# Optimization experiments

Hardware: AMD Instinct MI355X
Metric: run time of the kernel (lower is better)

The kernel has to match this reference:

```python
import jax, jax.numpy as jnp
import numpy as np

N_NODES = 50000
N_EDGES = 600000
D = 128
APPNP_K = 5
APPNP_ALPHA = 0.2


def _mish(x):
    return x * jnp.tanh(jax.nn.softplus(x))


def setup_inputs() -> dict:
    key = jax.random.key(0)
    ks = jax.random.split(key, 6)
    x = jax.random.normal(ks[0], (N_NODES, D), dtype=jnp.float32)
    src = jax.random.randint(ks[1], (N_EDGES,), 0, N_NODES, dtype=jnp.int32)
    dst = jax.random.randint(ks[2], (N_EDGES,), 0, N_NODES, dtype=jnp.int32)
    W1 = jax.random.normal(ks[3], (D, D), dtype=jnp.float32) * (1.0 / np.sqrt(D))
    b1 = jnp.zeros((D,), dtype=jnp.float32)
    W2 = jax.random.normal(ks[4], (2 * D, D), dtype=jnp.float32) * (1.0 / np.sqrt(2 * D))
    b2 = jnp.zeros((D,), dtype=jnp.float32)
    eps1 = jnp.zeros((1,), dtype=jnp.float32)
    eps2 = jnp.zeros((1,), dtype=jnp.float32)
    return {"x": x, "src": src, "dst": dst, "W1": W1, "b1": b1,
            "W2": W2, "b2": b2, "eps1": eps1, "eps2": eps2}


def _appnp(x0, src, dst):
    # DGL APPNPConv: symmetric degree normalization, k power-iteration steps.
    ones = jnp.ones((src.shape[0],), dtype=x0.dtype)
    deg_out = jnp.clip(jax.ops.segment_sum(ones, src, num_segments=N_NODES), 1.0)
    deg_in = jnp.clip(jax.ops.segment_sum(ones, dst, num_segments=N_NODES), 1.0)
    norm_o = deg_out[:, None] ** -0.5  # [N,1]
    norm_i = deg_in[:, None] ** -0.5
    h = x0
    for _ in range(APPNP_K):
        h = h * norm_o
        h = jax.ops.segment_sum(h[src], dst, num_segments=N_NODES)  # gather-scatter
        h = h * norm_i
        h = (1.0 - APPNP_ALPHA) * h + APPNP_ALPHA * x0
    return h


def _gin(h, src, dst, eps, W, b):
    # GINConv(sum, learn_eps): (1+eps)*h + sum_{j in N(i)} h_j, then Linear.
    agg = jax.ops.segment_sum(h[src], dst, num_segments=N_NODES)
    return ((1.0 + eps) * h + agg) @ W + b


def reference(x, src, dst, W1, b1, W2, b2, eps1, eps2):
    out = jnp.tanh(x)           # GCNNorm affects edge weights only; node feats then tanh
    x0 = out                    # res_out[0]
    out = _appnp(out, src, dst)
    out = _gin(out, src, dst, eps1[0], W1, b1)          # layer 0
    out = jnp.concatenate([out, x0], axis=1)            # residual concat
    out = _gin(out, src, dst, eps2[0], W2, b2)          # layer 1
    return _mish(out)
```

## Files before the change

### kernel.cpp

```cpp
#include <hip/hip_runtime.h>
#include <hip/hip_fp16.h>
#include <math.h>

#define NN 50000
#define NE 600000
#define NT ((NN + 31) / 32)

#define HB 64
#define HBINS 12500

typedef _Float16 half8_t __attribute__((ext_vector_type(8)));
typedef float f32x16 __attribute__((ext_vector_type(16)));
typedef float f32x2 __attribute__((ext_vector_type(2)));

union F2H { float2 f; __half2 h[2]; };

__device__ __forceinline__ float2 fp8_dec(unsigned short u) {
  f32x2 v = __builtin_amdgcn_cvt_pk_f32_fp8((unsigned int)u, false);
  float2 r; r.x = v.x; r.y = v.y; return r;
}
__device__ __forceinline__ unsigned short fp8_enc(float a, float b) {
  return (unsigned short)__builtin_amdgcn_cvt_pk_fp8_f32(a, b, 0u, false);
}


__global__ __launch_bounds__(256) void k_tanh(const float* __restrict__ x,
                                              const float* __restrict__ no,
                                              __half2* __restrict__ x0h,
                                              unsigned int* __restrict__ x0n8,
                                              unsigned int* __restrict__ x0p8) {
  int i = blockIdx.x * 256 + threadIdx.x;
  if (i >= NN * 32) return;
  float4 v = reinterpret_cast<const float4*>(x)[i];
  float t[4];
  float vv[4] = {v.x, v.y, v.z, v.w};
  #pragma unroll
  for (int j = 0; j < 4; ++j) {
    float xc = fminf(fmaxf(vv[j], -9.f), 9.f);
    float E = __expf(2.f * xc);
    t[j] = (E - 1.f) / (E + 1.f);
  }
  float s = no[i >> 5];
  F2H a;
  a.h[0] = __floats2half2_rn(t[0], t[1]);
  a.h[1] = __floats2half2_rn(t[2], t[3]);
  reinterpret_cast<float2*>(x0h)[i] = a.f;
  unsigned int p = __builtin_amdgcn_cvt_pk_fp8_f32(t[0] * s, t[1] * s, 0u, false);
  p = __builtin_amdgcn_cvt_pk_fp8_f32(t[2] * s, t[3] * s, p, true);
  x0n8[i] = p;
  unsigned int q = __builtin_amdgcn_cvt_pk_fp8_f32(t[0], t[1], 0u, false);
  q = __builtin_amdgcn_cvt_pk_fp8_f32(t[2], t[3], q, true);
  x0p8[i] = q;
}

__global__ __launch_bounds__(256) void k_wt(const float* __restrict__ W1,
                                            const float* __restrict__ W2,
                                            _Float16* __restrict__ w1p,
                                            _Float16* __restrict__ w2p) {
  int i = blockIdx.x * 256 + threadIdx.x;
  if (i < 128 * 128) {
    int k = i >> 7, n = i & 127;
    int nb = n >> 5, r = n & 31, ks = k >> 4, g = (k & 15) >> 3, j = k & 7;
    w1p[(((ks << 2) + nb) * 64 + (g << 5) + r) * 8 + j] = (_Float16)W1[i];
  } else {
    int q = i - 128 * 128;
    if (q < 256 * 128) {
      int k = q >> 7, n = q & 127;
      int nb = n >> 5, r = n & 31, ks = k >> 4, g = (k & 15) >> 3, j = k & 7;
      w2p[(((ks << 2) + nb) * 64 + (g << 5) + r) * 8 + j] = (_Float16)W2[q];
    }
  }
}

__global__ __launch_bounds__(1024) void k_hist(const int* __restrict__ src,
                                               const int* __restrict__ dst,
                                               int* __restrict__ hpart,
                                               int* __restrict__ lseq) {
  __shared__ int lh[HBINS];
  #pragma unroll 1
  for (int ph = 0; ph < 8; ++ph) {
    const int* idx = (ph & 4) ? dst : src;
    int base = (ph & 3) * HBINS;
    for (int i = threadIdx.x; i < HBINS; i += 1024) lh[i] = 0;
    __syncthreads();
    if (ph & 4) {
      for (int e = blockIdx.x * 1024 + threadIdx.x; e < NE; e += HB * 1024) {
        int v = idx[e] - base;
        if ((unsigned)v < (unsigned)HBINS) lseq[e] = atomicAdd(&lh[v], 1);
      }
    } else {
      for (int e = blockIdx.x * 1024 + threadIdx.x; e < NE; e += HB * 1024) {
        int v = idx[e] - base;
        if ((unsigned)v < (unsigned)HBINS) atomicAdd(&lh[v], 1);
      }
    }
    __syncthreads();
    int* outp = hpart + ((size_t)ph * HB + blockIdx.x) * HBINS;
    for (int i = threadIdx.x; i < HBINS; i += 1024) outp[i] = lh[i];
    __syncthreads();
  }
}

__global__ __launch_bounds__(256) void k_merge(int* __restrict__ hpart,
                                               int* __restrict__ ci,
                                               float* __restrict__ no,
                                               float* __restrict__ ni) {
  int i = blockIdx.x * 256 + threadIdx.x;
  if (i >= NN) return;
  int r = i / HBINS, bin = i - r * HBINS;
  const int* ps = hpart + ((size_t)(0 + r) * HB) * HBINS + bin;
  int* pd = hpart + ((size_t)(4 + r) * HB) * HBINS + bin;
  int so = 0, si = 0;
  #pragma unroll 8
  for (int b = 0; b < HB; ++b) so += ps[(size_t)b * HBINS];
  #pragma unroll 8
  for (int b = 0; b < HB; ++b) {
    int* p = pd + (size_t)b * HBINS;
    int t = *p;
    *p = si;
    si += t;
  }
  ci[i] = si;
  no[i] = rsqrtf((float)max(so, 1));
  ni[i] = rsqrtf((float)max(si, 1));
}

__global__ __launch_bounds__(1024) void k_scanA(const int* __restrict__ deg,
                                                int* __restrict__ incl,
                                                int* __restrict__ bsum) {
  int tid = threadIdx.x;
  int gid = blockIdx.x * 1024 + tid;
  int v = (gid < NN) ? deg[gid] : 0;
  int lane = tid & 63;
  #pragma unroll
  for (int o = 1; o < 64; o <<= 1) {
    int n = __shfl_up(v, o);
    if (lane >= o) v += n;
  }
  __shared__ int ws[16];
  int wid = tid >> 6;
  if (lane == 63) ws[wid] = v;
  __syncthreads();
  if (tid < 16) {
    int s = ws[tid];
    #pragma unroll
    for (int o = 1; o < 16; o <<= 1) {
      int n = __shfl_up(s, o);
      if (tid >= o) s += n;
    }
    ws[tid] = s;
  }
  __syncthreads();
  if (wid > 0) v += ws[wid - 1];
  if (gid < NN) incl[gid] = v;
  if (tid == 1023) bsum[blockIdx.x] = v;
}

__global__ __launch_bounds__(64) void k_scanB(const int* __restrict__ bsum,
                                              int* __restrict__ boff, int nb) {
  int t = threadIdx.x;
  int v = (t < nb) ? bsum[t] : 0;
  int orig = v;
  #pragma unroll
  for (int o = 1; o < 64; o <<= 1) {
    int n = __shfl_up(v, o);
    if (t >= o) v += n;
  }
  if (t < nb) boff[t] = v - orig;
}

__global__ __launch_bounds__(256) void k_scanC(const int* __restrict__ incl,
                                               const int* __restrict__ deg,
                                               const int* __restrict__ boff,
                                               int* __restrict__ rp) {
  int i = blockIdx.x * 256 + threadIdx.x;
  if (i < NN) rp[i] = incl[i] - deg[i] + boff[i >> 10];
  if (i == 0) rp[NN] = NE;
}

__global__ __launch_bounds__(256) void k_scatter(const int* __restrict__ src,
                                                 const int* __restrict__ dst,
                                                 const int* __restrict__ lseq,
                                                 const int* __restrict__ hpart,
                                                 const int* __restrict__ rp,
                                                 int* __restrict__ colsrc) {
  int e = blockIdx.x * 256 + threadIdx.x;
  if (e >= NE) return;
  int d = dst[e];
  int r = d / HBINS, bin = d - r * HBINS;
  int b = (e >> 10) & (HB - 1);
  int ofs = hpart[((size_t)(4 + r) * HB + b) * HBINS + bin];
  colsrc[rp[d] + ofs + lseq[e]] = src[e];
}

#define GATHER_LOOP(LOADEXPR)                                        \
  for (int base = 0; base < cnt; base += 64) {                      \
    int e = beg + base + lane;                                      \
    int cv = (e < end) ? cs[e] : 0;                                 \
    int m = cnt - base; if (m > 64) m = 64;                         \
    int j = 0;                                                      \
    for (; j + 8 <= m; j += 8) {                                    \
      _Pragma("unroll")                                             \
      for (int u = 0; u < 8; ++u) {                                 \
        int s = __builtin_amdgcn_readlane(cv, j + u);               \
        LOADEXPR;                                                   \
      }                                                             \
    }                                                               \
    if (j + 4 <= m) {                                               \
      _Pragma("unroll")                                             \
      for (int u = 0; u < 4; ++u) {                                 \
        int s = __builtin_amdgcn_readlane(cv, j + u);               \
        LOADEXPR;                                                   \
      }                                                             \
      j += 4;                                                       \
    }                                                               \
    if (j + 2 <= m) {                                               \
      _Pragma("unroll")                                             \
      for (int u = 0; u < 2; ++u) {                                 \
        int s = __builtin_amdgcn_readlane(cv, j + u);               \
        LOADEXPR;                                                   \
      }                                                             \
      j += 2;                                                       \
    }                                                               \
    if (j < m) {                                                    \
      int s = __builtin_amdgcn_readlane(cv, j);                     \
      LOADEXPR;                                                     \
    }                                                               \
  }

template <bool LAST>
__global__ __launch_bounds__(256) void k_appnp8(const unsigned short* __restrict__ h8,
                                                const __half2* __restrict__ x0,
                                                const float* __restrict__ no,
                                                const float* __restrict__ ni,
                                                const int* __restrict__ rp,
                                                const int* __restrict__ cs,
                                                unsigned short* __restrict__ out8,
                                                __half2* __restrict__ out16) {
  int w = (blockIdx.x * 256 + threadIdx.x) >> 6;
  int lane = threadIdx.x & 63;
  if (w >= NN) return;
  const unsigned short* hl = h8 + lane;
  int beg = rp[w], end = rp[w + 1], cnt = end - beg;
  float ax = 0.f, ay = 0.f;
  GATHER_LOOP({
    float2 f = fp8_dec(hl[s * 64]);
    ax += f.x; ay += f.y;
  })
  float wi = 0.8f * ni[w];
  float2 xv = __half22float2(x0[w * 64 + lane]);
  float rx = wi * ax + 0.2f * xv.x;
  float ry = wi * ay + 0.2f * xv.y;
  if (LAST) {
    out16[w * 64 + lane] = __floats2half2_rn(rx, ry);
  } else {
    float sc = no[w];
    out8[w * 64 + lane] = fp8_enc(rx * sc, ry * sc);
  }
}

__device__ inline void store_packed(_Float16* __restrict__ zp, int w, int lane,
                                    float v0, float v1) {
  int t = w >> 5, r = w & 31;
  int ks = lane >> 3, g = (lane >> 2) & 1, j = (lane & 3) * 2;
  size_t addr = (((size_t)t * 8 + ks) * 64 + g * 32 + r) * 8 + j;
  *reinterpret_cast<__half2*>(zp + addr) = __floats2half2_rn(v0, v1);
}

__global__ __launch_bounds__(256) void k_appnp_first8(const unsigned short* __restrict__ xn8,
                                                      const unsigned short* __restrict__ xp8,
                                                      const __half2* __restrict__ xp,
                                                      const float* __restrict__ epsp,
                                                      const float* __restrict__ no,
                                                      const float* __restrict__ ni,
                                                      const int* __restrict__ rp,
                                                      const int* __restrict__ cs,
                                                      unsigned short* __restrict__ hout8,
                                                      _Float16* __restrict__ zxout) {
  int w = (blockIdx.x * 256 + threadIdx.x) >> 6;
  int lane = threadIdx.x & 63;
  if (w >= NN) return;
  const unsigned short* xnl = xn8 + lane;
  const unsigned short* xpl = xp8 + lane;
  int beg = rp[w], end = rp[w + 1], cnt = end - beg;
  float ax = 0.f, ay = 0.f, bx = 0.f, by = 0.f;
  GATHER_LOOP({
    float2 f = fp8_dec(xnl[s * 64]);
    float2 g2 = fp8_dec(xpl[s * 64]);
    ax += f.x; ay += f.y; bx += g2.x; by += g2.y;
  })
  float2 xv = __half22float2(xp[w * 64 + lane]);
  float wi = 0.8f * ni[w];
  float sc = no[w];
  hout8[w * 64 + lane] = fp8_enc(sc * (wi * ax + 0.2f * xv.x),
                                 sc * (wi * ay + 0.2f * xv.y));
  float e2 = 1.0f + epsp[0];
  store_packed(zxout, w, lane, e2 * xv.x + bx, e2 * xv.y + by);
}

__global__ __launch_bounds__(256) void k_gather_z(const __half2* __restrict__ h,
                                                  const float* __restrict__ epsp,
                                                  const int* __restrict__ rp,
                                                  const int* __restrict__ cs,
                                                  _Float16* __restrict__ zout) {
  int w = (blockIdx.x * 256 + threadIdx.x) >> 6;
  int lane = threadIdx.x & 63;
  if (w >= NN) return;
  const __half2* hl = h + lane;
  int beg = rp[w], end = rp[w + 1], cnt = end - beg;
  float ax = 0.f, ay = 0.f;
  GATHER_LOOP({
    float2 f = __half22float2(hl[s * 64]);
    ax += f.x; ay += f.y;
  })
  float e1 = 1.0f + epsp[0];
  float2 hv = __half22float2(h[w * 64 + lane]);
  store_packed(zout, w, lane, e1 * hv.x + ax, e1 * hv.y + ay);
}

template <int KTOT, bool MISH>
__global__ __launch_bounds__(64) void k_mgemm(const _Float16* __restrict__ z0,
                                              const _Float16* __restrict__ z1,
                                              const _Float16* __restrict__ wp,
                                              const float* __restrict__ bias,
                                              float* __restrict__ outf,
                                              __half2* __restrict__ outh) {
  int lane = threadIdx.x;
  int t = blockIdx.x;
  int row0 = t * 32;
  if (row0 >= NN) return;
  int r31 = lane & 31, g = lane >> 5;
  f32x16 acc[4];
  #pragma unroll
  for (int i = 0; i < 4; ++i) acc[i] = (f32x16)(0.0f);
  #pragma unroll 4
  for (int ks = 0; ks < KTOT / 16; ++ks) {
    const _Float16* zp = (KTOT == 256 && ks >= 8) ? z1 : z0;
    int kls = (KTOT == 256) ? (ks & 7) : ks;
    half8_t a = *reinterpret_cast<const half8_t*>(
        zp + (((size_t)t * 8 + kls) * 64 + lane) * 8);
    #pragma unroll
    for (int nb = 0; nb < 4; ++nb) {
      half8_t b = *reinterpret_cast<const half8_t*>(
          wp + (((size_t)ks * 4 + nb) * 64 + lane) * 8);
      acc[nb] = __builtin_amdgcn_mfma_f32_32x32x16_f16(a, b, acc[nb], 0, 0, 0);
    }
  }
  #pragma unroll
  for (int nb = 0; nb < 4; ++nb) {
    float bv = bias[nb * 32 + r31];
    #pragma unroll
    for (int r = 0; r < 16; ++r) {
      int rl = (r & 3) + 8 * (r >> 2) + 4 * g;
      int grow = row0 + rl;
      if (grow < NN) {
        float v = acc[nb][r] + bv;
        if (MISH) {
          float E = __expf(v);
          float q = E * (E + 2.f);
          float mv = v * q / (q + 2.f);
          v = (v > 15.f) ? v : mv;
          outf[(size_t)grow * 128 + nb * 32 + r31] = v;
        } else {
          float u = __shfl_xor(v, 1);
          if (!(lane & 1)) {
            outh[((size_t)grow * 128 + nb * 32 + r31) >> 1] = __floats2half2_rn(v, u);
          }
        }
      }
    }
  }
}

extern "C" void kernel_launch(void* const* d_in, const int* in_sizes, int n_in,
                              void* d_out, int out_size, void* d_ws, size_t ws_size,
                              hipStream_t stream) {
  const float* x = (const float*)d_in[0];
  const int* src = (const int*)d_in[1];
  const int* dst = (const int*)d_in[2];
  const float* W1 = (const float*)d_in[3];
  const float* b1 = (const float*)d_in[4];
  const float* W2 = (const float*)d_in[5];
  const float* b2 = (const float*)d_in[6];
  const float* eps1 = (const float*)d_in[7];
  const float* eps2 = (const float*)d_in[8];
  float* out = (float*)d_out;

  char* ws = (char*)d_ws;
  size_t off = 0;
  auto alloc = [&](size_t bytes) -> void* {
    void* p = ws + off;
    off += (bytes + 255) & ~(size_t)255;
    return p;
  };
  const size_t NDP = (size_t)NT * 4096;
  __half2* x0h = (__half2*)alloc(NDP * 2);
  unsigned short* x0n8 = (unsigned short*)alloc(NDP);
  unsigned short* x0p8 = (unsigned short*)alloc(NDP);
  unsigned short* hA8 = (unsigned short*)alloc(NDP);
  unsigned short* hB8 = (unsigned short*)alloc(NDP);
  __half2* h5 = (__half2*)alloc(NDP * 2);
  __half2* zx = (__half2*)alloc(NDP * 2);
  __half2* z1p = (__half2*)alloc(NDP * 2);
  __half2* g1h = (__half2*)alloc(NDP * 2);
  __half2* zg = (__half2*)alloc(NDP * 2);
  _Float16* w1p = (_Float16*)alloc(128 * 128 * 2);
  _Float16* w2p = (_Float16*)alloc(256 * 128 * 2);
  int* ci = (int*)alloc(NN * 4);
  float* nrm_o = (float*)alloc(NN * 4);
  float* nrm_i = (float*)alloc(NN * 4);
  int* incl = (int*)alloc(NN * 4);
  int* bsum = (int*)alloc(64 * 4);
  int* boff = (int*)alloc(64 * 4);
  int* rp = (int*)alloc((NN + 1) * 4);
  int* lseq = (int*)alloc(NE * 4);
  int* colsrc = (int*)alloc(NE * 4);

  int* hpart = (int*)zx;

  k_hist<<<HB, 1024, 0, stream>>>(src, dst, hpart, lseq);
  k_merge<<<(NN + 255) / 256, 256, 0, stream>>>(hpart, ci, nrm_o, nrm_i);

  const int SB = (NN + 1023) / 1024;
  k_scanA<<<SB, 1024, 0, stream>>>(ci, incl, bsum);
  k_scanB<<<1, 64, 0, stream>>>(bsum, boff, SB);
  k_scanC<<<(NN + 255) / 256, 256, 0, stream>>>(incl, ci, boff, rp);
  const int EB = (NE + 255) / 256;
  k_scatter<<<EB, 256, 0, stream>>>(src, dst, lseq, hpart, rp, colsrc);

  k_tanh<<<(NN * 32 + 255) / 256, 256, 0, stream>>>(x, nrm_o, x0h,
                                                    (unsigned int*)x0n8,
                                                    (unsigned int*)x0p8);
  k_wt<<<192, 256, 0, stream>>>(W1, W2, w1p, w2p);

  const int GB = (NN * 64 + 255) / 256;
  k_appnp_first8<<<GB, 256, 0, stream>>>(x0n8, x0p8, x0h, eps2, nrm_o, nrm_i,
                                         rp, colsrc, hA8, (_Float16*)zx);
  k_appnp8<false><<<GB, 256, 0, stream>>>(hA8, x0h, nrm_o, nrm_i, rp, colsrc,
                                          hB8, nullptr);
  k_appnp8<false><<<GB, 256, 0, stream>>>(hB8, x0h, nrm_o, nrm_i, rp, colsrc,
                                          hA8, nullptr);
  k_appnp8<false><<<GB, 256, 0, stream>>>(hA8, x0h, nrm_o, nrm_i, rp, colsrc,
                                          hB8, nullptr);
  k_appnp8<true><<<GB, 256, 0, stream>>>(hB8, x0h, nrm_o, nrm_i, rp, colsrc,
                                         nullptr, h5);

  k_gather_z<<<GB, 256, 0, stream>>>(h5, eps1, rp, colsrc, (_Float16*)z1p);

  k_mgemm<128, false><<<NT, 64, 0, stream>>>((const _Float16*)z1p, nullptr, w1p, b1,
                                             nullptr, g1h);
  k_gather_z<<<GB, 256, 0, stream>>>(g1h, eps2, rp, colsrc, (_Float16*)zg);
  k_mgemm<256, true><<<NT, 64, 0, stream>>>((const _Float16*)zg, (const _Float16*)zx,
                                            w2p, b2, out, nullptr);
}
```

Measured before the change: 288.2 us.

## Pack two 16-bit degree counters per LDS word; split GIN gathers into feature halves

The histogram now packs counts for two node ranges into the high and low 16-bit halves of each shared-memory word. This covers all nodes in 2 passes instead of 8, reducing repeated edge-array reads and LDS zeroing, and the merge and scatter kernels are updated to unpack the halves. The GIN neighbour gather is split into two launches over feature halves, each wave handling two nodes with 32 lanes apiece, so each gathered row is 128 bytes and the per-launch working set is smaller. The risk is 16-bit counter overflow if any per-block count reaches 65536, plus divergence and wasted lanes when the two paired nodes have very different degrees.

```diff
diff --git a/kernel.cpp b/kernel.cpp
--- a/kernel.cpp
+++ b/kernel.cpp
@@ -7,7 +7,7 @@
 #define NT ((NN + 31) / 32)
 
 #define HB 64
-#define HBINS 12500
+#define NBIN2 25000
 
 typedef _Float16 half8_t __attribute__((ext_vector_type(8)));
 typedef float f32x16 __attribute__((ext_vector_type(16)));
@@ -72,57 +72,65 @@
   }
 }
 
-__global__ __launch_bounds__(1024) void k_hist(const int* __restrict__ src,
-                                               const int* __restrict__ dst,
-                                               int* __restrict__ hpart,
-                                               int* __restrict__ lseq) {
-  __shared__ int lh[HBINS];
+__global__ __launch_bounds__(1024) void k_hist2(const int* __restrict__ src,
+                                                const int* __restrict__ dst,
+                                                unsigned int* __restrict__ hpart,
+                                                int* __restrict__ lseq) {
+  __shared__ unsigned int lh[NBIN2];
   #pragma unroll 1
-  for (int ph = 0; ph < 8; ++ph) {
-    const int* idx = (ph & 4) ? dst : src;
-    int base = (ph & 3) * HBINS;
-    for (int i = threadIdx.x; i < HBINS; i += 1024) lh[i] = 0;
+  for (int ph = 0; ph < 2; ++ph) {
+    const int* idx = ph ? dst : src;
+    for (int i = threadIdx.x; i < NBIN2; i += 1024) lh[i] = 0;
     __syncthreads();
-    if (ph & 4) {
+    if (ph) {
       for (int e = blockIdx.x * 1024 + threadIdx.x; e < NE; e += HB * 1024) {
-        int v = idx[e] - base;
-        if ((unsigned)v < (unsigned)HBINS) lseq[e] = atomicAdd(&lh[v], 1);
+        int v = idx[e];
+        int hi = (v >= NBIN2) ? 1 : 0;
+        int bin = v - hi * NBIN2;
+        unsigned int old = atomicAdd(&lh[bin], hi ? 65536u : 1u);
+        lseq[e] = (int)((old >> (hi * 16)) & 0xffffu);
       }
     } else {
       for (int e = blockIdx.x * 1024 + threadIdx.x; e < NE; e += HB * 1024) {
-        int v = idx[e] - base;
-        if ((unsigned)v < (unsigned)HBINS) atomicAdd(&lh[v], 1);
+        int v = idx[e];
+        int hi = (v >= NBIN2) ? 1 : 0;
+        atomicAdd(&lh[v - hi * NBIN2], hi ? 65536u : 1u);
       }
     }
     __syncthreads();
-    int* outp = hpart + ((size_t)ph * HB + blockIdx.x) * HBINS;
-    for (int i = threadIdx.x; i < HBINS; i += 1024) outp[i] = lh[i];
+    unsigned int* outp = hpart + ((size_t)ph * HB + blockIdx.x) * NBIN2;
+    for (int i = threadIdx.x; i < NBIN2; i += 1024) outp[i] = lh[i];
     __syncthreads();
   }
 }
 
-__global__ __launch_bounds__(256) void k_merge(int* __restrict__ hpart,
-                                               int* __restrict__ ci,
-                                               float* __restrict__ no,
-                                               float* __restrict__ ni) {
-  int i = blockIdx.x * 256 + threadIdx.x;
-  if (i >= NN) return;
-  int r = i / HBINS, bin = i - r * HBINS;
-  const int* ps = hpart + ((size_t)(0 + r) * HB) * HBINS + bin;
-  int* pd = hpart + ((size_t)(4 + r) * HB) * HBINS + bin;
-  int so = 0, si = 0;
-  #pragma unroll 8
-  for (int b = 0; b < HB; ++b) so += ps[(size_t)b * HBINS];
+__global__ __launch_bounds__(256) void k_merge2(unsigned int* __restrict__ hpart,
+                                                int* __restrict__ ci,
+                                                float* __restrict__ no,
+                                                float* __restrict__ ni) {
+  int bin = blockIdx.x * 256 + threadIdx.x;
+  if (bin >= NBIN2) return;
+  const unsigned int* ps = hpart + bin;
+  unsigned int* pd = hpart + (size_t)HB * NBIN2 + bin;
+  unsigned int so0 = 0, so1 = 0, si0 = 0, si1 = 0;
   #pragma unroll 8
   for (int b = 0; b < HB; ++b) {
-    int* p = pd + (size_t)b * HBINS;
-    int t = *p;
-    *p = si;
-    si += t;
-  }
-  ci[i] = si;
-  no[i] = rsqrtf((float)max(so, 1));
-  ni[i] = rsqrtf((float)max(si, 1));
+    unsigned int v = ps[(size_t)b * NBIN2];
+    so0 += v & 0xffffu; so1 += v >> 16;
+  }
+  #pragma unroll 8
+  for (int b = 0; b < HB; ++b) {
+    unsigned int* p = pd + (size_t)b * NBIN2;
+    unsigned int v = *p;
+    *p = si0 | (si1 << 16);
+    si0 += v & 0xffffu; si1 += v >> 16;
+  }
+  ci[bin] = (int)si0;
+  ci[bin + NBIN2] = (int)si1;
+  no[bin] = rsqrtf((float)max((int)so0, 1));
+  no[bin + NBIN2] = rsqrtf((float)max((int)so1, 1));
+  ni[bin] = rsqrtf((float)max((int)si0, 1));
+  ni[bin + NBIN2] = rsqrtf((float)max((int)si1, 1));
 }
 
 __global__ __launch_bounds__(1024) void k_scanA(const int* __restrict__ deg,
@@ -181,15 +189,17 @@
 __global__ __launch_bounds__(256) void k_scatter(const int* __restrict__ src,
                                                  const int* __restrict__ dst,
                                                  const int* __restrict__ lseq,
-                                                 const int* __restrict__ hpart,
+                                                 const unsigned int* __restrict__ hpart,
                                                  const int* __restrict__ rp,
                                                  int* __restrict__ colsrc) {
   int e = blockIdx.x * 256 + threadIdx.x;
   if (e >= NE) return;
   int d = dst[e];
-  int r = d / HBINS, bin = d - r * HBINS;
+  int hi = (d >= NBIN2) ? 1 : 0;
+  int bin = d - hi * NBIN2;
   int b = (e >> 10) & (HB - 1);
-  int ofs = hpart[((size_t)(4 + r) * HB + b) * HBINS + bin];
+  unsigned int w = hpart[((size_t)HB + b) * NBIN2 + bin];
+  int ofs = (int)((w >> (hi * 16)) & 0xffffu);
   colsrc[rp[d] + ofs + lseq[e]] = src[e];
 }
 
@@ -298,24 +308,47 @@
   store_packed(zxout, w, lane, e2 * xv.x + bx, e2 * xv.y + by);
 }
 
-__global__ __launch_bounds__(256) void k_gather_z(const __half2* __restrict__ h,
-                                                  const float* __restrict__ epsp,
-                                                  const int* __restrict__ rp,
-                                                  const int* __restrict__ cs,
-                                                  _Float16* __restrict__ zout) {
-  int w = (blockIdx.x * 256 + threadIdx.x) >> 6;
+__global__ __launch_bounds__(256) void k_gz_pair(const __half2* __restrict__ h,
+                                                 const float* __restrict__ epsp,
+                                                 const int* __restrict__ rp,
+                                                 const int* __restrict__ cs,
+                                                 _Float16* __restrict__ zout,
+                                                 int hf) {
+  int wp = (blockIdx.x * 256 + threadIdx.x) >> 6;
+  if (wp >= NN / 2) return;
   int lane = threadIdx.x & 63;
-  if (w >= NN) return;
-  const __half2* hl = h + lane;
+  int l31 = lane & 31;
+  int w = wp * 2 + (lane >> 5);
+  const __half2* hl = h + hf * 32 + l31;
   int beg = rp[w], end = rp[w + 1], cnt = end - beg;
   float ax = 0.f, ay = 0.f;
-  GATHER_LOOP({
-    float2 f = __half22float2(hl[s * 64]);
-    ax += f.x; ay += f.y;
-  })
+  for (int base = 0;; base += 32) {
+    int m = cnt - base;
+    if (m > 32) m = 32;
+    int mA = __shfl(m, 0), mB = __shfl(m, 32);
+    int mmax = mA > mB ? mA : mB;
+    if (mmax <= 0) break;
+    int cv = (base + l31 < cnt) ? cs[beg + base + l31] : 0;
+    int j = 0;
+#define PSTEP(U) { int s = __shfl(cv, j + (U), 32);                    \
+                   float2 f = __half22float2(hl[(size_t)s * 64]);      \
+                   if (j + (U) < m) { ax += f.x; ay += f.y; } }
+    for (; j + 8 <= mmax; j += 8) {
+      PSTEP(0) PSTEP(1) PSTEP(2) PSTEP(3) PSTEP(4) PSTEP(5) PSTEP(6) PSTEP(7)
+    }
+    if (j + 4 <= mmax) { PSTEP(0) PSTEP(1) PSTEP(2) PSTEP(3) j += 4; }
+    if (j + 2 <= mmax) { PSTEP(0) PSTEP(1) j += 2; }
+    if (j < mmax) { PSTEP(0) }
+#undef PSTEP
+  }
   float e1 = 1.0f + epsp[0];
-  float2 hv = __half22float2(h[w * 64 + lane]);
-  store_packed(zout, w, lane, e1 * hv.x + ax, e1 * hv.y + ay);
+  float2 hv = __half22float2(h[(size_t)w * 64 + hf * 32 + l31]);
+  int k0 = hf * 64 + l31 * 2;
+  int t = w >> 5, r = w & 31;
+  int ks = k0 >> 4, g = (k0 >> 3) & 1, jj = k0 & 7;
+  size_t addr = (((size_t)t * 8 + ks) * 64 + g * 32 + r) * 8 + jj;
+  *reinterpret_cast<__half2*>(zout + addr) =
+      __floats2half2_rn(e1 * hv.x + ax, e1 * hv.y + ay);
 }
 
 template <int KTOT, bool MISH>
@@ -416,10 +449,10 @@
   int* lseq = (int*)alloc(NE * 4);
   int* colsrc = (int*)alloc(NE * 4);
 
-  int* hpart = (int*)zx;
-
-  k_hist<<<HB, 1024, 0, stream>>>(src, dst, hpart, lseq);
-  k_merge<<<(NN + 255) / 256, 256, 0, stream>>>(hpart, ci, nrm_o, nrm_i);
+  unsigned int* hpart = (unsigned int*)zx;
+
+  k_hist2<<<HB, 1024, 0, stream>>>(src, dst, hpart, lseq);
+  k_merge2<<<(NBIN2 + 255) / 256, 256, 0, stream>>>(hpart, ci, nrm_o, nrm_i);
 
   const int SB = (NN + 1023) / 1024;
   k_scanA<<<SB, 1024, 0, stream>>>(ci, incl, bsum);
@@ -434,6 +467,7 @@
   k_wt<<<192, 256, 0, stream>>>(W1, W2, w1p, w2p);
 
   const int GB = (NN * 64 + 255) / 256;
+  const int GP = (NN / 2 * 64 + 255) / 256;
   k_appnp_first8<<<GB, 256, 0, stream>>>(x0n8, x0p8, x0h, eps2, nrm_o, nrm_i,
                                          rp, colsrc, hA8, (_Float16*)zx);
   k_appnp8<false><<<GB, 256, 0, stream>>>(hA8, x0h, nrm_o, nrm_i, rp, colsrc,
@@ -445,11 +479,13 @@
   k_appnp8<true><<<GB, 256, 0, stream>>>(hB8, x0h, nrm_o, nrm_i, rp, colsrc,
                                          nullptr, h5);
 
-  k_gather_z<<<GB, 256, 0, stream>>>(h5, eps1, rp, colsrc, (_Float16*)z1p);
+  k_gz_pair<<<GP, 256, 0, stream>>>(h5, eps1, rp, colsrc, (_Float16*)z1p, 0);
+  k_gz_pair<<<GP, 256, 0, stream>>>(h5, eps1, rp, colsrc, (_Float16*)z1p, 1);
 
   k_mgemm<128, false><<<NT, 64, 0, stream>>>((const _Float16*)z1p, nullptr, w1p, b1,
                                              nullptr, g1h);
-  k_gather_z<<<GB, 256, 0, stream>>>(g1h, eps2, rp, colsrc, (_Float16*)zg);
+  k_gz_pair<<<GP, 256, 0, stream>>>(g1h, eps2, rp, colsrc, (_Float16*)zg, 0);
+  k_gz_pair<<<GP, 256, 0, stream>>>(g1h, eps2, rp, colsrc, (_Float16*)zg, 1);
   k_mgemm<256, true><<<NT, 64, 0, stream>>>((const _Float16*)zg, (const _Float16*)zx,
                                             w2p, b2, out, nullptr);
 }
```

Result: faster. 275.4 us (median of 2 runs) (-4.4%).
